# Performance work log

Measured on AMD Instinct MI355X. Metric: run time of the kernel, lower is better.

Reference implementation:

```python
import jax, jax.numpy as jnp
import numpy as np

N_EMBD = 126
N_HEADS = 6
HEAD_DIM = N_EMBD // N_HEADS  # 21


def setup_inputs() -> dict:
    key = jax.random.key(0)
    k1, k2, k3 = jax.random.split(key, 3)
    B, T = 8, 2048
    x = jax.random.normal(k1, (B, T, N_EMBD), dtype=jnp.float32)
    # torch Linear weights stored as (out, in); we store transposed (in, out) for x @ W
    w_attn = jax.random.normal(k2, (N_EMBD, 3 * N_EMBD), dtype=jnp.float32) * (1.0 / np.sqrt(N_EMBD))
    w_proj = jax.random.normal(k3, (N_EMBD, N_EMBD), dtype=jnp.float32) * (1.0 / np.sqrt(N_EMBD))
    return {"x": x, "w_attn": w_attn, "w_proj": w_proj}


def reference(x, w_attn, w_proj):
    B, T, C = x.shape
    qkv = x @ w_attn                      # [B, T, 3C]
    q, k, v = jnp.split(qkv, 3, axis=-1)  # each [B, T, C]

    def heads(t):  # [B,T,C] -> [B,H,T,hd]
        return t.reshape(B, T, N_HEADS, HEAD_DIM).transpose(0, 2, 1, 3)

    q, k, v = heads(q), heads(k), heads(v)
    scale = 1.0 / np.sqrt(HEAD_DIM).astype(np.float32)
    scores = jnp.einsum('bhqd,bhkd->bhqk', q, k) * scale  # [B,H,T,T]
    causal = jnp.tril(jnp.ones((T, T), dtype=bool))
    scores = jnp.where(causal, scores, jnp.finfo(scores.dtype).min)
    attn = jax.nn.softmax(scores, axis=-1)
    out = jnp.einsum('bhqk,bhkd->bhqd', attn, v)           # [B,H,T,hd]
    out = out.transpose(0, 2, 1, 3).reshape(B, T, C)
    return out @ w_proj
```

## Files before the change

kernel.cpp:

```cpp
#include <hip/hip_runtime.h>
#include <hip/hip_bf16.h>


#define B_ 8
#define T_ 2048
#define C_ 126
#define H_ 6
#define D_ 21
#define TC_ 378
#define KP_ 128
#define DP_ 32
#define M_ 16384

typedef __hip_bfloat16 bf16;
typedef __bf16 bf16_t;
typedef __bf16 bf16x8 __attribute__((ext_vector_type(8)));
typedef float f32x4 __attribute__((ext_vector_type(4)));

__device__ __forceinline__ float ldf(const bf16* p, long i) { return __bfloat162float(p[i]); }
__device__ __forceinline__ float ldf(const float* p, long i) { return p[i]; }
__device__ __forceinline__ void stf(bf16* p, long i, float v) { p[i] = __float2bfloat16(v); }
__device__ __forceinline__ void stf(float* p, long i, float v) { p[i] = v; }

__global__ void sniff_kernel(const unsigned int* __restrict__ xw,
                             int* __restrict__ flag) {
  const int tid = threadIdx.x;
  const unsigned int w = xw[tid * 97 + 13];
  const unsigned int e = (w >> 7) & 0xFF;
  const bool bflike = (e >= 115 && e <= 131) || ((w & 0x7FFFu) == 0);
  const unsigned long long mask = __ballot(bflike);
  if (tid == 0) *flag = (__popcll(mask) >= 40) ? 1 : 0;
}

template <typename T>
__device__ __forceinline__ void prep_w_body(const T* __restrict__ wa,
                                            const T* __restrict__ wp,
                                            bf16_t* __restrict__ WTa,
                                            bf16_t* __restrict__ WTp) {
  const int stride = gridDim.x * blockDim.x;
  const int idx0 = blockIdx.x * blockDim.x + threadIdx.x;
  for (int i = idx0; i < 384 * KP_ + KP_ * KP_; i += stride) {
    if (i < 384 * KP_) {
      const int n = i >> 7, k = i & 127;
      WTa[i] = (k < C_ && n < TC_) ? (bf16_t)ldf(wa, (long)k * TC_ + n) : (bf16_t)0.f;
    } else {
      const int j = i - 384 * KP_;
      const int n = j >> 7, k = j & 127;
      WTp[j] = (k < C_ && n < C_) ? (bf16_t)ldf(wp, (long)k * C_ + n) : (bf16_t)0.f;
    }
  }
}

__global__ __launch_bounds__(256) void prep_w_kernel(
    const void* __restrict__ wa, const void* __restrict__ wp,
    bf16_t* __restrict__ WTa, bf16_t* __restrict__ WTp,
    const int* __restrict__ flag) {
  if (*flag) prep_w_body<bf16>((const bf16*)wa, (const bf16*)wp, WTa, WTp);
  else       prep_w_body<float>((const float*)wa, (const float*)wp, WTa, WTp);
}

#define QS_ 40

template <typename T>
__device__ __forceinline__ void qkv_body(
    const T* __restrict__ x, const bf16_t* __restrict__ WT,
    bf16_t* __restrict__ Qb, bf16_t* __restrict__ Kb, bf16_t* __restrict__ VT,
    bf16_t* __restrict__ xs, bf16_t* __restrict__ qbuf,
    bf16_t* __restrict__ kbuf, bf16_t* __restrict__ vbuf) {
  const int m0 = blockIdx.x * 16;
  const int tid = threadIdx.x;
  for (int i = tid; i < 16 * KP_; i += 256) {
    const int row = i >> 7, col = i & 127;
    xs[i] = (col < C_) ? (bf16_t)ldf(x, (long)(m0 + row) * C_ + col) : (bf16_t)0.f;
  }
  for (int i = tid; i < 6 * 16 * 11; i += 256) {
    const int h = i / 176, rem = i - h * 176, t = rem / 11, d = 21 + rem % 11;
    qbuf[(h * 16 + t) * QS_ + d] = (bf16_t)0.f;
    kbuf[(h * 16 + t) * QS_ + d] = (bf16_t)0.f;
  }
  for (int i = tid; i < 6 * 11 * 16; i += 256) {
    const int h = i / 176, rem = i - h * 176, d = 21 + rem / 16, t = rem % 16;
    vbuf[(h * 32 + d) * 16 + t] = (d == 21) ? (bf16_t)1.f : (bf16_t)0.f;
  }
  __syncthreads();

  const int wv = tid >> 6, lane = tid & 63;
  const int lr = lane & 15, quad = lane >> 4;
  const bf16_t* ar = xs + lr * KP_ + quad * 8;
  const bf16x8 a0 = *(const bf16x8*)(ar);
  const bf16x8 a1 = *(const bf16x8*)(ar + 32);
  const bf16x8 a2 = *(const bf16x8*)(ar + 64);
  const bf16x8 a3 = *(const bf16x8*)(ar + 96);

  for (int nt = wv; nt < 24; nt += 4) {
    const int n0 = nt * 16;
    const bf16x8* bp = (const bf16x8*)(WT + (long)(n0 + lr) * KP_ + quad * 8);
    f32x4 acc = {0.f, 0.f, 0.f, 0.f};
    acc = __builtin_amdgcn_mfma_f32_16x16x32_bf16(a0, bp[0],  acc, 0, 0, 0);
    acc = __builtin_amdgcn_mfma_f32_16x16x32_bf16(a1, bp[4],  acc, 0, 0, 0);
    acc = __builtin_amdgcn_mfma_f32_16x16x32_bf16(a2, bp[8],  acc, 0, 0, 0);
    acc = __builtin_amdgcn_mfma_f32_16x16x32_bf16(a3, bp[12], acc, 0, 0, 0);

    const int c = n0 + lr;
    if (c < TC_) {
      const int which = c / C_;
      const int cc = c - which * C_;
      const int h = cc / D_, d = cc - h * D_;
#pragma unroll
      for (int r = 0; r < 4; ++r) {
        const int t = quad * 4 + r;
        if (which == 0)
          qbuf[(h * 16 + t) * QS_ + d] = (bf16_t)(acc[r] * 0.21821789023599236f);
        else if (which == 1)
          kbuf[(h * 16 + t) * QS_ + d] = (bf16_t)acc[r];
        else
          vbuf[(h * 32 + d) * 16 + t] = (bf16_t)acc[r];
      }
    }
  }
  __syncthreads();

  const int b = m0 >> 11, t0 = m0 & 2047;
  for (int i = tid; i < 192; i += 256) {
    const int j = (i < 96) ? i : i - 96;
    const int h = j >> 4, t = j & 15;
    const int4* src = (const int4*)(((i < 96) ? qbuf : kbuf) + (h * 16 + t) * QS_);
    int4* dst = (int4*)((((i < 96) ? Qb : Kb)) + ((long)(b * H_ + h) * T_ + (t0 + t)) * DP_);
    dst[0] = src[0]; dst[1] = src[1]; dst[2] = src[2]; dst[3] = src[3];
  }
  for (int i = tid; i < 192; i += 256) {
    const int h = i >> 5, d = i & 31;
    const int4* src = (const int4*)(vbuf + (h * 32 + d) * 16);
    int4* dst = (int4*)(VT + ((long)(b * H_ + h) * DP_ + d) * T_ + t0);
    dst[0] = src[0]; dst[1] = src[1];
  }
}

__global__ __launch_bounds__(256) void qkv_mfma(
    const void* __restrict__ x, const bf16_t* __restrict__ WT,
    bf16_t* __restrict__ Qb, bf16_t* __restrict__ Kb, bf16_t* __restrict__ VT,
    const int* __restrict__ flag) {
  __shared__ __align__(16) bf16_t xs[16 * KP_];
  __shared__ __align__(16) bf16_t qbuf[6 * 16 * QS_];
  __shared__ __align__(16) bf16_t kbuf[6 * 16 * QS_];
  __shared__ __align__(16) bf16_t vbuf[6 * 32 * 16];
  if (*flag) qkv_body<bf16>((const bf16*)x, WT, Qb, Kb, VT, xs, qbuf, kbuf, vbuf);
  else       qkv_body<float>((const float*)x, WT, Qb, Kb, VT, xs, qbuf, kbuf, vbuf);
}

__global__ __launch_bounds__(256, 8) void attn_mfma(
    const bf16_t* __restrict__ Qb, const bf16_t* __restrict__ Kb,
    const bf16_t* __restrict__ VT, bf16_t* __restrict__ ATTp) {
  __shared__ __align__(16) float smem[4352];
  const int bh = blockIdx.x;
  const int pr = blockIdx.y;
  const int tid = threadIdx.x;
  const int wv = tid >> 6, lane = tid & 63;
  const int lr = lane & 15, quad = lane >> 4;
  const int q0 = pr * 32;
  const int mq = quad * 4;

  const bf16_t* Qbh = Qb + (long)bh * T_ * DP_;
  const bf16_t* Kbh = Kb + (long)bh * T_ * DP_;
  const bf16_t* VTbh = VT + (long)bh * DP_ * T_;

  const bf16x8 qf0 = *(const bf16x8*)(Qbh + (long)(q0 + lr) * DP_ + quad * 8);
  const bf16x8 qf1 = *(const bf16x8*)(Qbh + (long)(q0 + 16 + lr) * DP_ + quad * 8);

  f32x4 o00 = {0.f,0.f,0.f,0.f}, o01 = {0.f,0.f,0.f,0.f};
  f32x4 o10 = {0.f,0.f,0.f,0.f}, o11 = {0.f,0.f,0.f,0.f};
  bf16_t* pl0 = (bf16_t*)smem + wv * 1024;
  bf16_t* pl1 = pl0 + 512;
  const int rsw = ((lane ^ (lane >> 2)) << 3);

  for (int t = wv; t <= pr; t += 4) {
    const int kb = t * 32;
    const bf16x8 k0 = *(const bf16x8*)(Kbh + (long)(kb + lr) * DP_ + quad * 8);
    const bf16x8 k1 = *(const bf16x8*)(Kbh + (long)(kb + 16 + lr) * DP_ + quad * 8);
    f32x4 s00 = {0.f,0.f,0.f,0.f}, s01 = {0.f,0.f,0.f,0.f};
    f32x4 s10 = {0.f,0.f,0.f,0.f}, s11 = {0.f,0.f,0.f,0.f};
    s00 = __builtin_amdgcn_mfma_f32_16x16x32_bf16(qf0, k0, s00, 0, 0, 0);
    s01 = __builtin_amdgcn_mfma_f32_16x16x32_bf16(qf0, k1, s01, 0, 0, 0);
    s10 = __builtin_amdgcn_mfma_f32_16x16x32_bf16(qf1, k0, s10, 0, 0, 0);
    s11 = __builtin_amdgcn_mfma_f32_16x16x32_bf16(qf1, k1, s11, 0, 0, 0);

    if (t == pr) {
#pragma unroll
      for (int r = 0; r < 4; ++r) {
        if (lr > mq + r) { s00[r] = -1e30f; s11[r] = -1e30f; }
        s01[r] = -1e30f;
      }
    }
#pragma unroll
    for (int r = 0; r < 4; ++r) {
      const float p00 = __expf(s00[r]);
      const float p01 = __expf(s01[r]);
      const float p10 = __expf(s10[r]);
      const float p11 = __expf(s11[r]);
      const int b0 = ((lr >> 3) << 4) + mq + r;
      const int b1 = b0 + 32;
      const int i0 = ((b0 ^ (b0 >> 2)) << 3) + (lr & 7);
      const int i1 = ((b1 ^ (b1 >> 2)) << 3) + (lr & 7);
      pl0[i0] = (bf16_t)p00;
      pl0[i1] = (bf16_t)p01;
      pl1[i0] = (bf16_t)p10;
      pl1[i1] = (bf16_t)p11;
    }
    __builtin_amdgcn_wave_barrier();
    const bf16x8 pf0 = *(const bf16x8*)(pl0 + rsw);
    const bf16x8 pf1 = *(const bf16x8*)(pl1 + rsw);
    __builtin_amdgcn_wave_barrier();

    const bf16x8 v0 = *(const bf16x8*)(VTbh + (long)lr * T_ + kb + quad * 8);
    const bf16x8 v1 = *(const bf16x8*)(VTbh + (long)(16 + lr) * T_ + kb + quad * 8);
    o00 = __builtin_amdgcn_mfma_f32_16x16x32_bf16(pf0, v0, o00, 0, 0, 0);
    o01 = __builtin_amdgcn_mfma_f32_16x16x32_bf16(pf0, v1, o01, 0, 0, 0);
    o10 = __builtin_amdgcn_mfma_f32_16x16x32_bf16(pf1, v0, o10, 0, 0, 0);
    o11 = __builtin_amdgcn_mfma_f32_16x16x32_bf16(pf1, v1, o11, 0, 0, 0);
  }

  __syncthreads();
  {
    float* my = smem + (wv * 64 + lane) * 17;
#pragma unroll
    for (int j = 0; j < 4; ++j) {
      my[j]      = o00[j];
      my[4 + j]  = o01[j];
      my[8 + j]  = o10[j];
      my[12 + j] = o11[j];
    }
  }
  __syncthreads();

  if (wv == 0) {
    float tot[16];
#pragma unroll
    for (int j = 0; j < 16; ++j)
      tot[j] = smem[lane * 17 + j] + smem[(64 + lane) * 17 + j] +
               smem[(128 + lane) * 17 + j] + smem[(192 + lane) * 17 + j];
    const int b = bh / H_, h = bh - b * H_;
#pragma unroll
    for (int r = 0; r < 4; ++r) {
      const float rl0 = 1.f / __shfl(tot[4 + r],  (lane & 48) + 5, 64);
      const float rl1 = 1.f / __shfl(tot[12 + r], (lane & 48) + 5, 64);
      const int qA = q0 + mq + r, qB = qA + 16;
      bf16_t* opA = ATTp + (long)(b * T_ + qA) * KP_ + h * D_;
      bf16_t* opB = ATTp + (long)(b * T_ + qB) * KP_ + h * D_;
      opA[lr] = (bf16_t)(tot[r] * rl0);
      opB[lr] = (bf16_t)(tot[8 + r] * rl1);
      if (lr < 5) {
        opA[16 + lr] = (bf16_t)(tot[4 + r] * rl0);
        opB[16 + lr] = (bf16_t)(tot[12 + r] * rl1);
      }
    }
  }
}

__global__ __launch_bounds__(256) void proj_mfma(
    const bf16_t* __restrict__ ATTp, const bf16_t* __restrict__ WT,
    void* __restrict__ out, const int* __restrict__ flag) {
  const int m0 = blockIdx.x * 16;
  const int tid = threadIdx.x;
  const int wv = tid >> 6, lane = tid & 63;
  const int lr = lane & 15, quad = lane >> 4;
  const int isbf = *flag;

  const bf16x8* ap = (const bf16x8*)(ATTp + (long)(m0 + lr) * KP_ + quad * 8);
  const bf16x8 a0 = ap[0], a1 = ap[4], a2 = ap[8], a3 = ap[12];

  for (int nt = wv; nt < 8; nt += 4) {
    const int n0 = nt * 16;
    const bf16x8* bp = (const bf16x8*)(WT + (long)(n0 + lr) * KP_ + quad * 8);
    f32x4 acc = {0.f, 0.f, 0.f, 0.f};
    acc = __builtin_amdgcn_mfma_f32_16x16x32_bf16(a0, bp[0],  acc, 0, 0, 0);
    acc = __builtin_amdgcn_mfma_f32_16x16x32_bf16(a1, bp[4],  acc, 0, 0, 0);
    acc = __builtin_amdgcn_mfma_f32_16x16x32_bf16(a2, bp[8],  acc, 0, 0, 0);
    acc = __builtin_amdgcn_mfma_f32_16x16x32_bf16(a3, bp[12], acc, 0, 0, 0);

    const int c = n0 + lr;
    if (c < C_) {
#pragma unroll
      for (int r = 0; r < 4; ++r) {
        const int m = m0 + quad * 4 + r;
        if (isbf) stf((bf16*)out,  (long)m * C_ + c, acc[r]);
        else      stf((float*)out, (long)m * C_ + c, acc[r]);
      }
    }
  }
}

extern "C" void kernel_launch(void* const* d_in, const int* in_sizes, int n_in,
                              void* d_out, int out_size, void* d_ws, size_t ws_size,
                              hipStream_t stream) {
  const void* x      = d_in[0];
  const void* w_attn = d_in[1];
  const void* w_proj = d_in[2];

  char* base = (char*)d_ws;
  int* flag = (int*)base;
  const long QKV = (long)48 * T_ * DP_;
  bf16_t* Qb = (bf16_t*)(base + 256);
  bf16_t* Kb = Qb + QKV;
  bf16_t* VT = Kb + QKV;
  bf16_t* WTa  = VT + QKV;
  bf16_t* WTp  = WTa + 384 * KP_;
  bf16_t* ATTp = WTp + KP_ * KP_;

  sniff_kernel<<<1, 64, 0, stream>>>((const unsigned int*)x, flag);
  prep_w_kernel<<<64, 256, 0, stream>>>(w_attn, w_proj, WTa, WTp, flag);
  qkv_mfma<<<M_ / 16, 256, 0, stream>>>(x, WTa, Qb, Kb, VT, flag);
  attn_mfma<<<dim3(48, 64), 256, 0, stream>>>(Qb, Kb, VT, ATTp);
  proj_mfma<<<M_ / 16, 256, 0, stream>>>(ATTp, WTp, d_out, flag);
}
```

Measured before the change: 139.4 us.

## Prefetch K/V tiles, fold dtype sniff into kernels, use exp2 scaling

Several changes at once. The attention loop now loads the next K/V tile into registers while the current one is computed, and the query scale gains a log2(e) factor so the softmax can call exp2f instead of __expf. Query tiles are launched in reverse order so the heaviest causal blocks start first, and the launch-bounds occupancy hint drops from 8 to 6. The separate dtype-sniff kernel is removed, each kernel probes the input dtype itself, and x is loaded two elements at a time. The costs are extra registers for the prefetched tiles and a redundant probe in every block.

```diff
diff --git a/kernel.cpp b/kernel.cpp
--- a/kernel.cpp
+++ b/kernel.cpp
@@ -11,6 +11,7 @@
 #define KP_ 128
 #define DP_ 32
 #define M_ 16384
+#define QSCALE 0.31481923469333463f
 
 typedef __hip_bfloat16 bf16;
 typedef __bf16 bf16_t;
@@ -22,14 +23,25 @@
 __device__ __forceinline__ void stf(bf16* p, long i, float v) { p[i] = __float2bfloat16(v); }
 __device__ __forceinline__ void stf(float* p, long i, float v) { p[i] = v; }
 
-__global__ void sniff_kernel(const unsigned int* __restrict__ xw,
-                             int* __restrict__ flag) {
-  const int tid = threadIdx.x;
-  const unsigned int w = xw[tid * 97 + 13];
-  const unsigned int e = (w >> 7) & 0xFF;
-  const bool bflike = (e >= 115 && e <= 131) || ((w & 0x7FFFu) == 0);
-  const unsigned long long mask = __ballot(bflike);
-  if (tid == 0) *flag = (__popcll(mask) >= 40) ? 1 : 0;
+__device__ __forceinline__ unsigned int ld2(const bf16* x, long i) {
+  return *(const unsigned int*)((const unsigned short*)x + i);
+}
+__device__ __forceinline__ unsigned int ld2(const float* x, long i) {
+  const float2 f = *(const float2*)(x + i);
+  union { bf16_t b[2]; unsigned int u; } cv;
+  cv.b[0] = (bf16_t)f.x; cv.b[1] = (bf16_t)f.y;
+  return cv.u;
+}
+
+__device__ __forceinline__ void probe_dtype(const void* x, int tid, int* sflag) {
+  if (tid < 64) {
+    const unsigned int w = ((const unsigned int*)x)[tid * 97 + 13];
+    const unsigned int e = (w >> 7) & 0xFF;
+    const bool bflike = (e >= 115 && e <= 131) || ((w & 0x7FFFu) == 0);
+    const unsigned long long mask = __ballot(bflike);
+    if (tid == 0) *sflag = (__popcll(mask) >= 40) ? 1 : 0;
+  }
+  __syncthreads();
 }
 
 template <typename T>
@@ -52,10 +64,12 @@
 }
 
 __global__ __launch_bounds__(256) void prep_w_kernel(
-    const void* __restrict__ wa, const void* __restrict__ wp,
-    bf16_t* __restrict__ WTa, bf16_t* __restrict__ WTp,
-    const int* __restrict__ flag) {
-  if (*flag) prep_w_body<bf16>((const bf16*)wa, (const bf16*)wp, WTa, WTp);
+    const void* __restrict__ x, const void* __restrict__ wa,
+    const void* __restrict__ wp, bf16_t* __restrict__ WTa,
+    bf16_t* __restrict__ WTp) {
+  __shared__ int sflag;
+  probe_dtype(x, threadIdx.x, &sflag);
+  if (sflag) prep_w_body<bf16>((const bf16*)wa, (const bf16*)wp, WTa, WTp);
   else       prep_w_body<float>((const float*)wa, (const float*)wp, WTa, WTp);
 }
 
@@ -69,9 +83,11 @@
     bf16_t* __restrict__ kbuf, bf16_t* __restrict__ vbuf) {
   const int m0 = blockIdx.x * 16;
   const int tid = threadIdx.x;
-  for (int i = tid; i < 16 * KP_; i += 256) {
-    const int row = i >> 7, col = i & 127;
-    xs[i] = (col < C_) ? (bf16_t)ldf(x, (long)(m0 + row) * C_ + col) : (bf16_t)0.f;
+  for (int i = tid; i < 16 * 64; i += 256) {
+    const int row = i >> 6, cp = i & 63;
+    unsigned int v = 0;
+    if (cp < 63) v = ld2(x, (long)(m0 + row) * C_ + 2 * cp);
+    ((unsigned int*)xs)[i] = v;
   }
   for (int i = tid; i < 6 * 16 * 11; i += 256) {
     const int h = i / 176, rem = i - h * 176, t = rem / 11, d = 21 + rem % 11;
@@ -110,7 +126,7 @@
       for (int r = 0; r < 4; ++r) {
         const int t = quad * 4 + r;
         if (which == 0)
-          qbuf[(h * 16 + t) * QS_ + d] = (bf16_t)(acc[r] * 0.21821789023599236f);
+          qbuf[(h * 16 + t) * QS_ + d] = (bf16_t)(acc[r] * QSCALE);
         else if (which == 1)
           kbuf[(h * 16 + t) * QS_ + d] = (bf16_t)acc[r];
         else
@@ -138,22 +154,23 @@
 
 __global__ __launch_bounds__(256) void qkv_mfma(
     const void* __restrict__ x, const bf16_t* __restrict__ WT,
-    bf16_t* __restrict__ Qb, bf16_t* __restrict__ Kb, bf16_t* __restrict__ VT,
-    const int* __restrict__ flag) {
+    bf16_t* __restrict__ Qb, bf16_t* __restrict__ Kb, bf16_t* __restrict__ VT) {
   __shared__ __align__(16) bf16_t xs[16 * KP_];
   __shared__ __align__(16) bf16_t qbuf[6 * 16 * QS_];
   __shared__ __align__(16) bf16_t kbuf[6 * 16 * QS_];
   __shared__ __align__(16) bf16_t vbuf[6 * 32 * 16];
-  if (*flag) qkv_body<bf16>((const bf16*)x, WT, Qb, Kb, VT, xs, qbuf, kbuf, vbuf);
+  __shared__ int sflag;
+  probe_dtype(x, threadIdx.x, &sflag);
+  if (sflag) qkv_body<bf16>((const bf16*)x, WT, Qb, Kb, VT, xs, qbuf, kbuf, vbuf);
   else       qkv_body<float>((const float*)x, WT, Qb, Kb, VT, xs, qbuf, kbuf, vbuf);
 }
 
-__global__ __launch_bounds__(256, 8) void attn_mfma(
+__global__ __launch_bounds__(256, 6) void attn_mfma(
     const bf16_t* __restrict__ Qb, const bf16_t* __restrict__ Kb,
     const bf16_t* __restrict__ VT, bf16_t* __restrict__ ATTp) {
   __shared__ __align__(16) float smem[4352];
   const int bh = blockIdx.x;
-  const int pr = blockIdx.y;
+  const int pr = 63 - blockIdx.y;
   const int tid = threadIdx.x;
   const int wv = tid >> 6, lane = tid & 63;
   const int lr = lane & 15, quad = lane >> 4;
@@ -173,16 +190,32 @@
   bf16_t* pl1 = pl0 + 512;
   const int rsw = ((lane ^ (lane >> 2)) << 3);
 
+  bf16x8 kc0, kc1, vc0, vc1;
+  if (wv <= pr) {
+    const int kb = wv * 32;
+    kc0 = *(const bf16x8*)(Kbh + (long)(kb + lr) * DP_ + quad * 8);
+    kc1 = *(const bf16x8*)(Kbh + (long)(kb + 16 + lr) * DP_ + quad * 8);
+    vc0 = *(const bf16x8*)(VTbh + (long)lr * T_ + kb + quad * 8);
+    vc1 = *(const bf16x8*)(VTbh + (long)(16 + lr) * T_ + kb + quad * 8);
+  }
+
   for (int t = wv; t <= pr; t += 4) {
-    const int kb = t * 32;
-    const bf16x8 k0 = *(const bf16x8*)(Kbh + (long)(kb + lr) * DP_ + quad * 8);
-    const bf16x8 k1 = *(const bf16x8*)(Kbh + (long)(kb + 16 + lr) * DP_ + quad * 8);
+    bf16x8 kn0, kn1, vn0, vn1;
+    const int tn = t + 4;
+    if (tn <= pr) {
+      const int kbn = tn * 32;
+      kn0 = *(const bf16x8*)(Kbh + (long)(kbn + lr) * DP_ + quad * 8);
+      kn1 = *(const bf16x8*)(Kbh + (long)(kbn + 16 + lr) * DP_ + quad * 8);
+      vn0 = *(const bf16x8*)(VTbh + (long)lr * T_ + kbn + quad * 8);
+      vn1 = *(const bf16x8*)(VTbh + (long)(16 + lr) * T_ + kbn + quad * 8);
+    }
+
     f32x4 s00 = {0.f,0.f,0.f,0.f}, s01 = {0.f,0.f,0.f,0.f};
     f32x4 s10 = {0.f,0.f,0.f,0.f}, s11 = {0.f,0.f,0.f,0.f};
-    s00 = __builtin_amdgcn_mfma_f32_16x16x32_bf16(qf0, k0, s00, 0, 0, 0);
-    s01 = __builtin_amdgcn_mfma_f32_16x16x32_bf16(qf0, k1, s01, 0, 0, 0);
-    s10 = __builtin_amdgcn_mfma_f32_16x16x32_bf16(qf1, k0, s10, 0, 0, 0);
-    s11 = __builtin_amdgcn_mfma_f32_16x16x32_bf16(qf1, k1, s11, 0, 0, 0);
+    s00 = __builtin_amdgcn_mfma_f32_16x16x32_bf16(qf0, kc0, s00, 0, 0, 0);
+    s01 = __builtin_amdgcn_mfma_f32_16x16x32_bf16(qf0, kc1, s01, 0, 0, 0);
+    s10 = __builtin_amdgcn_mfma_f32_16x16x32_bf16(qf1, kc0, s10, 0, 0, 0);
+    s11 = __builtin_amdgcn_mfma_f32_16x16x32_bf16(qf1, kc1, s11, 0, 0, 0);
 
     if (t == pr) {
 #pragma unroll
@@ -193,10 +226,10 @@
     }
 #pragma unroll
     for (int r = 0; r < 4; ++r) {
-      const float p00 = __expf(s00[r]);
-      const float p01 = __expf(s01[r]);
-      const float p10 = __expf(s10[r]);
-      const float p11 = __expf(s11[r]);
+      const float p00 = exp2f(s00[r]);
+      const float p01 = exp2f(s01[r]);
+      const float p10 = exp2f(s10[r]);
+      const float p11 = exp2f(s11[r]);
       const int b0 = ((lr >> 3) << 4) + mq + r;
       const int b1 = b0 + 32;
       const int i0 = ((b0 ^ (b0 >> 2)) << 3) + (lr & 7);
@@ -211,12 +244,12 @@
     const bf16x8 pf1 = *(const bf16x8*)(pl1 + rsw);
     __builtin_amdgcn_wave_barrier();
 
-    const bf16x8 v0 = *(const bf16x8*)(VTbh + (long)lr * T_ + kb + quad * 8);
-    const bf16x8 v1 = *(const bf16x8*)(VTbh + (long)(16 + lr) * T_ + kb + quad * 8);
-    o00 = __builtin_amdgcn_mfma_f32_16x16x32_bf16(pf0, v0, o00, 0, 0, 0);
-    o01 = __builtin_amdgcn_mfma_f32_16x16x32_bf16(pf0, v1, o01, 0, 0, 0);
-    o10 = __builtin_amdgcn_mfma_f32_16x16x32_bf16(pf1, v0, o10, 0, 0, 0);
-    o11 = __builtin_amdgcn_mfma_f32_16x16x32_bf16(pf1, v1, o11, 0, 0, 0);
+    o00 = __builtin_amdgcn_mfma_f32_16x16x32_bf16(pf0, vc0, o00, 0, 0, 0);
+    o01 = __builtin_amdgcn_mfma_f32_16x16x32_bf16(pf0, vc1, o01, 0, 0, 0);
+    o10 = __builtin_amdgcn_mfma_f32_16x16x32_bf16(pf1, vc0, o10, 0, 0, 0);
+    o11 = __builtin_amdgcn_mfma_f32_16x16x32_bf16(pf1, vc1, o11, 0, 0, 0);
+
+    kc0 = kn0; kc1 = kn1; vc0 = vn0; vc1 = vn1;
   }
 
   __syncthreads();
@@ -257,13 +290,16 @@
 }
 
 __global__ __launch_bounds__(256) void proj_mfma(
-    const bf16_t* __restrict__ ATTp, const bf16_t* __restrict__ WT,
-    void* __restrict__ out, const int* __restrict__ flag) {
+    const void* __restrict__ x, const bf16_t* __restrict__ ATTp,
+    const bf16_t* __restrict__ WT, void* __restrict__ out) {
+  __shared__ int sflag;
+  probe_dtype(x, threadIdx.x, &sflag);
+  const int isbf = sflag;
+
   const int m0 = blockIdx.x * 16;
   const int tid = threadIdx.x;
   const int wv = tid >> 6, lane = tid & 63;
   const int lr = lane & 15, quad = lane >> 4;
-  const int isbf = *flag;
 
   const bf16x8* ap = (const bf16x8*)(ATTp + (long)(m0 + lr) * KP_ + quad * 8);
   const bf16x8 a0 = ap[0], a1 = ap[4], a2 = ap[8], a3 = ap[12];
@@ -297,7 +333,6 @@
   const void* w_proj = d_in[2];
 
   char* base = (char*)d_ws;
-  int* flag = (int*)base;
   const long QKV = (long)48 * T_ * DP_;
   bf16_t* Qb = (bf16_t*)(base + 256);
   bf16_t* Kb = Qb + QKV;
@@ -306,9 +341,8 @@
   bf16_t* WTp  = WTa + 384 * KP_;
   bf16_t* ATTp = WTp + KP_ * KP_;
 
-  sniff_kernel<<<1, 64, 0, stream>>>((const unsigned int*)x, flag);
-  prep_w_kernel<<<64, 256, 0, stream>>>(w_attn, w_proj, WTa, WTp, flag);
-  qkv_mfma<<<M_ / 16, 256, 0, stream>>>(x, WTa, Qb, Kb, VT, flag);
+  prep_w_kernel<<<64, 256, 0, stream>>>(x, w_attn, w_proj, WTa, WTp);
+  qkv_mfma<<<M_ / 16, 256, 0, stream>>>(x, WTa, Qb, Kb, VT);
   attn_mfma<<<dim3(48, 64), 256, 0, stream>>>(Qb, Kb, VT, ATTp);
-  proj_mfma<<<M_ / 16, 256, 0, stream>>>(ATTp, WTp, d_out, flag);
-}
+  proj_mfma<<<M_ / 16, 256, 0, stream>>>(x, ATTp, WTp, d_out);
+}
```

Result: slower. 165.0 us (+18.4%).
